# Kernel optimization log

Measured on AMD Instinct MI355X. Metric: run time of the kernel, lower is better.

Reference implementation:

```python
import jax, jax.numpy as jnp
import numpy as np

D = 256        # feature dim
H = 8          # num_heads
HD = D // H    # head dim = 32
G = 16         # graphs in batch
NA = 128       # nodes per graph, side A
NB = 128       # nodes per graph, side B


def setup_inputs() -> dict:
    key = jax.random.key(0)
    ks = jax.random.split(key, 7)
    s = 1.0 / np.sqrt(D)
    A = jax.random.normal(ks[0], (G * NA, D), dtype=jnp.float32)
    B = jax.random.normal(ks[1], (G * NB, D), dtype=jnp.float32)
    batch1 = jnp.repeat(jnp.arange(G, dtype=jnp.int64), NA)
    batch2 = jnp.repeat(jnp.arange(G, dtype=jnp.int64), NB)
    W1 = jax.random.normal(ks[2], (D, D), dtype=jnp.float32) * s
    bias1 = jax.random.normal(ks[3], (D,), dtype=jnp.float32) * s
    W2 = jax.random.normal(ks[4], (D, D), dtype=jnp.float32) * s
    bias2 = jax.random.normal(ks[5], (D,), dtype=jnp.float32) * s
    q = jax.random.normal(ks[6], (HD,), dtype=jnp.float32) * s
    return {"A": A, "batch1": batch1, "B": B, "batch2": batch2,
            "W1": W1, "bias1": bias1, "W2": W2, "bias2": bias2, "q": q}


def reference(A, batch1, B, batch2, W1, bias1, W2, bias2, q):
    # equal-size graphs: counts are uniform, so torch.split == reshape
    g = int(np.asarray(batch1)[-1]) + 1
    nA = A.shape[0] // g
    nB = B.shape[0] // g
    x1 = A @ W1.T + bias1            # [g*nA, D]
    x2 = B @ W2.T + bias2            # [g*nB, D]
    # faithful to torch: raw C-order view [nA, D] -> [H, nA, HD]
    x1 = x1.reshape(g, H, nA, HD)    # [g, H, nA, hd]
    x2 = x2.reshape(g, H, nB, HD)    # [g, H, nB, hd]
    # att[g,h,i,j] = sum_k tanh(x1[g,h,i,k] * x2[g,h,j,k]) * q[k]
    att = jnp.einsum('ghijk,k->ghij',
                     jnp.tanh(x1[:, :, :, None, :] * x2[:, :, None, :, :]), q)
    b2a = jax.nn.softmax(att.mean(axis=3), axis=2)   # [g, H, nA]
    a2b = jax.nn.softmax(att.mean(axis=2), axis=2)   # [g, H, nB]
    A_p = jnp.einsum('ghik,ghi->ghk', x1, b2a).reshape(g, D)
    B_p = jnp.einsum('ghjk,ghj->ghk', x2, a2b).reshape(g, D)
    return jnp.concatenate([A_p, B_p], axis=1)       # [g, 2D]
```

## Files before the change

### kernel.cpp

```cpp
#include <hip/hip_runtime.h>

#define C2L2E 2.8853900817779268f
#define LOG2E 1.4426950408889634f

#define WS_X1   0
#define WS_X2   524288
#define WS_RS   1048576
#define WS_CP   1064960
#define WS_AH   1114112
#define WS_AL   1376256
#define WS_BH   1638400
#define WS_BL   1900544
#define WS_W1H  2162688
#define WS_W1L  2195456
#define WS_W2H  2228224
#define WS_W2L  2260992

#define L_SMAT 0
#define L_COLP 8448
#define L_RED8 8960
#define L_X2   9216
#define L_X1   13312

typedef short bf16x8 __attribute__((ext_vector_type(8)));
typedef float f32x4 __attribute__((ext_vector_type(4)));

__device__ __forceinline__ int swz4(int row, int c4) { return (c4 ^ (row & 7)) << 2; }

__device__ __forceinline__ unsigned short bf16rne(float f) {
    unsigned u = __float_as_uint(f);
    u += 0x7FFF + ((u >> 16) & 1);
    return (unsigned short)(u >> 16);
}
__device__ __forceinline__ float bf16tof(unsigned short h) {
    return __uint_as_float(((unsigned)h) << 16);
}

__global__ __launch_bounds__(512) void k0_convert(
        const float* __restrict__ A, const float* __restrict__ B,
        const float* __restrict__ W1, const float* __restrict__ W2,
        float* __restrict__ ws) {
    const int idx = blockIdx.x * 512 + threadIdx.x;
    const float* src; unsigned short *dh, *dl; int base;
    if (idx < 131072)      { src = A;  dh = (unsigned short*)(ws + WS_AH);  dl = (unsigned short*)(ws + WS_AL);  base = idx; }
    else if (idx < 262144) { src = B;  dh = (unsigned short*)(ws + WS_BH);  dl = (unsigned short*)(ws + WS_BL);  base = idx - 131072; }
    else if (idx < 278528) { src = W1; dh = (unsigned short*)(ws + WS_W1H); dl = (unsigned short*)(ws + WS_W1L); base = idx - 262144; }
    else                   { src = W2; dh = (unsigned short*)(ws + WS_W2H); dl = (unsigned short*)(ws + WS_W2L); base = idx - 278528; }
    float4 v = ((const float4*)src)[base];
    ushort4 h, l;
    h.x = bf16rne(v.x); l.x = bf16rne(v.x - bf16tof(h.x));
    h.y = bf16rne(v.y); l.y = bf16rne(v.y - bf16tof(h.y));
    h.z = bf16rne(v.z); l.z = bf16rne(v.z - bf16tof(h.z));
    h.w = bf16rne(v.w); l.w = bf16rne(v.w - bf16tof(h.w));
    ((ushort4*)dh)[base] = h;
    ((ushort4*)dl)[base] = l;
}

__global__ __launch_bounds__(256) void k1_mfma(
        const float* __restrict__ b1, const float* __restrict__ b2,
        float* __restrict__ ws) {
    const int bid = blockIdx.x, tid = threadIdx.x;
    const int mat = bid >> 7, idx = bid & 127;
    const int r0 = (idx >> 2) * 64, c0 = (idx & 3) * 64;
    const unsigned short* IH = (const unsigned short*)(ws + (mat ? WS_BH : WS_AH));
    const unsigned short* IL = (const unsigned short*)(ws + (mat ? WS_BL : WS_AL));
    const unsigned short* WH = (const unsigned short*)(ws + (mat ? WS_W2H : WS_W1H));
    const unsigned short* WL = (const unsigned short*)(ws + (mat ? WS_W2L : WS_W1L));
    const float* bs = mat ? b2 : b1;
    float* xo = ws + (mat ? WS_X2 : WS_X1);

    const int wv = tid >> 6, lane = tid & 63;
    const int l16 = lane & 15, khi = (lane >> 4) * 8;
    const int row = r0 + wv * 16 + l16;

    f32x4 acc[4];
    #pragma unroll
    for (int nt = 0; nt < 4; ++nt) acc[nt] = (f32x4){0.f, 0.f, 0.f, 0.f};

    const unsigned short* ihp = IH + (size_t)row * 256 + khi;
    const unsigned short* ilp = IL + (size_t)row * 256 + khi;

    for (int kt = 0; kt < 8; ++kt) {
        bf16x8 ah = *(const bf16x8*)(ihp + kt * 32);
        bf16x8 al = *(const bf16x8*)(ilp + kt * 32);
        #pragma unroll
        for (int nt = 0; nt < 4; ++nt) {
            const int cB = c0 + nt * 16 + l16;
            bf16x8 wh = *(const bf16x8*)(WH + (size_t)cB * 256 + kt * 32 + khi);
            bf16x8 wl = *(const bf16x8*)(WL + (size_t)cB * 256 + kt * 32 + khi);
            acc[nt] = __builtin_amdgcn_mfma_f32_16x16x32_bf16(ah, wh, acc[nt], 0, 0, 0);
            acc[nt] = __builtin_amdgcn_mfma_f32_16x16x32_bf16(ah, wl, acc[nt], 0, 0, 0);
            acc[nt] = __builtin_amdgcn_mfma_f32_16x16x32_bf16(al, wh, acc[nt], 0, 0, 0);
        }
    }

    const int rowb = r0 + wv * 16 + (lane >> 4) * 4;
    #pragma unroll
    for (int nt = 0; nt < 4; ++nt) {
        const int col = c0 + nt * 16 + l16;
        const float bb = bs[col];
        #pragma unroll
        for (int rg = 0; rg < 4; ++rg)
            xo[(size_t)(rowb + rg) * 256 + col] = acc[nt][rg] + bb;
    }
}

__global__ __launch_bounds__(512) void k2_att(
        float* __restrict__ ws, const float* __restrict__ q) {
    __shared__ float sm[15360];
    const int tid = threadIdx.x;
    const int gh = blockIdx.x >> 1, s = blockIdx.x & 1;
    float* x2L = sm + L_X2;
    float* x1L = sm + L_X1;

    {
        const float4* src2 = (const float4*)(ws + WS_X2 + (size_t)gh * 4096);
        #pragma unroll
        for (int p = 0; p < 2; ++p) {
            int n = tid + p * 512;
            float4 v = src2[n];
            int ni = n >> 3, c4 = n & 7;
            *(float4*)(x2L + ni * 32 + swz4(ni, c4)) = v;
        }
        const float4* src1 = (const float4*)(ws + WS_X1 + (size_t)gh * 4096 + s * 2048);
        float4 v = src1[tid];
        int nl = tid >> 3, c4 = tid & 7;
        *(float4*)(x1L + nl * 32 + swz4(nl, c4)) = v;
    }
    __syncthreads();

    {
        const int j = tid & 127, iset = tid >> 7;
        float xr[32], qt[32];
        #pragma unroll
        for (int cc = 0; cc < 8; ++cc) {
            float4 v = *(float4*)(x2L + j * 32 + swz4(j, cc));
            xr[cc*4+0] = v.x * C2L2E; xr[cc*4+1] = v.y * C2L2E;
            xr[cc*4+2] = v.z * C2L2E; xr[cc*4+3] = v.w * C2L2E;
            float4 qv = *(const float4*)(q + cc * 4);
            qt[cc*4+0] = -2.f * qv.x; qt[cc*4+1] = -2.f * qv.y;
            qt[cc*4+2] = -2.f * qv.z; qt[cc*4+3] = -2.f * qv.w;
        }
        float colacc = 0.f;
        for (int rr = 0; rr < 16; ++rr) {
            const int r = iset * 16 + rr;
            float a[32];
            #pragma unroll
            for (int cc = 0; cc < 8; ++cc) {
                float4 v = *(float4*)(x1L + r * 32 + swz4(r, cc));
                a[cc*4+0] = v.x; a[cc*4+1] = v.y; a[cc*4+2] = v.z; a[cc*4+3] = v.w;
            }
            float S0 = 0.f, S1 = 0.f;
            #pragma unroll
            for (int kp = 0; kp < 16; ++kp) {
                float p0 = a[2*kp]   * xr[2*kp];
                float p1 = a[2*kp+1] * xr[2*kp+1];
                float d0 = __builtin_amdgcn_exp2f(fminf(p0, 60.f)) + 1.f;
                float d1 = __builtin_amdgcn_exp2f(fminf(p1, 60.f)) + 1.f;
                float rD = __builtin_amdgcn_rcpf(d0 * d1);
                float U  = fmaf(qt[2*kp+1], d0, qt[2*kp] * d1);
                if (kp & 1) S1 = fmaf(U, rD, S1); else S0 = fmaf(U, rD, S0);
            }
            float S = S0 + S1;
            colacc += S;
            sm[L_SMAT + r * 132 + j] = S;
        }
        sm[L_COLP + iset * 128 + j] = colacc;
    }
    __syncthreads();

    if (tid < 256) {
        const int row = tid >> 2, seg = tid & 3;
        float acc = 0.f;
        #pragma unroll
        for (int m = 0; m < 8; ++m) {
            float4 v = *(float4*)(sm + L_SMAT + row * 132 + seg * 32 + m * 4);
            acc += (v.x + v.y) + (v.z + v.w);
        }
        sm[L_RED8 + row * 4 + seg] = acc;
    }
    __syncthreads();
    if (tid < 64) {
        float v = sm[L_RED8 + tid*4] + sm[L_RED8 + tid*4+1]
                + sm[L_RED8 + tid*4+2] + sm[L_RED8 + tid*4+3];
        ws[WS_RS + gh * 128 + s * 64 + tid] = v;
    } else if (tid < 192) {
        const int j = tid - 64;
        ws[WS_CP + (size_t)(gh * 2 + s) * 128 + j] =
            sm[L_COLP + j] + sm[L_COLP + 128 + j] + sm[L_COLP + 256 + j] + sm[L_COLP + 384 + j];
    }
}

__global__ __launch_bounds__(256) void kb_finish(
        const float* __restrict__ ws, float* __restrict__ out) {
    const int gh = blockIdx.x;
    const int g = gh >> 3, h = gh & 7;
    const int tid = threadIdx.x;
    const int side = tid >> 7;
    const int u = tid & 127;
    const int w2 = (u >> 6) & 1;
    const int lane = tid & 63;

    __shared__ float warr[2][128];
    __shared__ float red[4];
    __shared__ float red2[4];
    __shared__ float part[2][4][32];

    float m;
    if (side == 0) {
        m = ws[WS_RS + gh * 128 + u] * 0.0078125f;
    } else {
        m = (ws[WS_CP + (size_t)(gh * 2 + 0) * 128 + u] +
             ws[WS_CP + (size_t)(gh * 2 + 1) * 128 + u]) * 0.0078125f;
    }

    float mx = m;
    #pragma unroll
    for (int d = 32; d >= 1; d >>= 1) mx = fmaxf(mx, __shfl_xor(mx, d));
    if (lane == 0) red[side * 2 + w2] = mx;
    __syncthreads();
    mx = fmaxf(red[side * 2], red[side * 2 + 1]);

    float e = __builtin_amdgcn_exp2f((m - mx) * LOG2E);
    float sme = e;
    #pragma unroll
    for (int d = 32; d >= 1; d >>= 1) sme += __shfl_xor(sme, d);
    if (lane == 0) red2[side * 2 + w2] = sme;
    __syncthreads();
    const float tot = red2[side * 2] + red2[side * 2 + 1];
    warr[side][u] = e * __builtin_amdgcn_rcpf(tot);
    __syncthreads();

    const int k = u & 31, is = u >> 5;
    const float* xt = ws + (side ? WS_X2 : WS_X1) + (size_t)gh * 4096;
    float p = 0.f;
    #pragma unroll 4
    for (int r = 0; r < 32; ++r)
        p = fmaf(xt[(is * 32 + r) * 32 + k], warr[side][is * 32 + r], p);
    part[side][is][k] = p;
    __syncthreads();
    if (u < 32 && side == 0) {
        float o = part[0][0][u] + part[0][1][u] + part[0][2][u] + part[0][3][u];
        out[(size_t)g * 512 + h * 32 + u] = o;
    } else if (u < 32 && side == 1) {
        float o = part[1][0][u] + part[1][1][u] + part[1][2][u] + part[1][3][u];
        out[(size_t)g * 512 + 256 + h * 32 + u] = o;
    }
}

extern "C" void kernel_launch(void* const* d_in, const int* in_sizes, int n_in,
                              void* d_out, int out_size, void* d_ws, size_t ws_size,
                              hipStream_t stream) {
    const float* A  = (const float*)d_in[0];
    const float* B  = (const float*)d_in[2];
    const float* W1 = (const float*)d_in[4];
    const float* b1 = (const float*)d_in[5];
    const float* W2 = (const float*)d_in[6];
    const float* b2 = (const float*)d_in[7];
    const float* q  = (const float*)d_in[8];
    float* ws  = (float*)d_ws;
    float* out = (float*)d_out;

    k0_convert<<<576, 512, 0, stream>>>(A, B, W1, W2, ws);
    k1_mfma<<<256, 256, 0, stream>>>(b1, b2, ws);
    k2_att<<<256, 512, 0, stream>>>(ws, q);
    kb_finish<<<128, 256, 0, stream>>>(ws, out);
}
```

Baseline: 45.38 us.

## Fuse attention and softmax-finish kernels, pre-tile bf16 operands into MFMA fragment layout

The attention and finish kernels are merged into one 1024-thread block per (graph, head). It computes the full 128x128 score tile, does the row and column softmax, and forms the weighted sums from the x1/x2 tiles already in shared memory. This removes one launch and the global round trip for the partial row and column sums. The convert kernel now writes A/B/W hi/lo bf16 data in MFMA-fragment order, so the GEMM reads each fragment as one contiguous 16-byte per-lane load. The trade-off is half as many blocks (128 instead of 256) with larger shared memory, which may lower occupancy during the tanh-heavy phase.

```diff
diff --git a/kernel.cpp b/kernel.cpp
--- a/kernel.cpp
+++ b/kernel.cpp
@@ -5,27 +5,33 @@
 
 #define WS_X1   0
 #define WS_X2   524288
-#define WS_RS   1048576
-#define WS_CP   1064960
-#define WS_AH   1114112
-#define WS_AL   1376256
-#define WS_BH   1638400
-#define WS_BL   1900544
-#define WS_W1H  2162688
-#define WS_W1L  2195456
-#define WS_W2H  2228224
-#define WS_W2L  2260992
-
-#define L_SMAT 0
-#define L_COLP 8448
-#define L_RED8 8960
-#define L_X2   9216
-#define L_X1   13312
+#define WS_AH   1048576
+#define WS_AL   1310720
+#define WS_BH   1572864
+#define WS_BL   1835008
+#define WS_W1H  2097152
+#define WS_W1L  2129920
+#define WS_W2H  2162688
+#define WS_W2L  2195456
+
+#define L_X2    0
+#define L_X1    4096
+#define L_SMAT  8192
+#define L_COLP  25088
+#define L_RED8  27136
+#define L_RSUM  28160
+#define L_CSUM  28288
+#define L_WARR  28416
+#define L_REDM  28672
+#define L_PART  28680
 
 typedef short bf16x8 __attribute__((ext_vector_type(8)));
 typedef float f32x4 __attribute__((ext_vector_type(4)));
 
 __device__ __forceinline__ int swz4(int row, int c4) { return (c4 ^ (row & 7)) << 2; }
+__device__ __forceinline__ int swzf(int row, int k) {
+    return (((k >> 2) ^ (row & 7)) << 2) | (k & 3);
+}
 
 __device__ __forceinline__ unsigned short bf16rne(float f) {
     unsigned u = __float_as_uint(f);
@@ -36,24 +42,34 @@
     return __uint_as_float(((unsigned)h) << 16);
 }
 
-__global__ __launch_bounds__(512) void k0_convert(
+__global__ __launch_bounds__(256) void k0_convert(
         const float* __restrict__ A, const float* __restrict__ B,
         const float* __restrict__ W1, const float* __restrict__ W2,
         float* __restrict__ ws) {
-    const int idx = blockIdx.x * 512 + threadIdx.x;
-    const float* src; unsigned short *dh, *dl; int base;
-    if (idx < 131072)      { src = A;  dh = (unsigned short*)(ws + WS_AH);  dl = (unsigned short*)(ws + WS_AL);  base = idx; }
-    else if (idx < 262144) { src = B;  dh = (unsigned short*)(ws + WS_BH);  dl = (unsigned short*)(ws + WS_BL);  base = idx - 131072; }
-    else if (idx < 278528) { src = W1; dh = (unsigned short*)(ws + WS_W1H); dl = (unsigned short*)(ws + WS_W1L); base = idx - 262144; }
-    else                   { src = W2; dh = (unsigned short*)(ws + WS_W2H); dl = (unsigned short*)(ws + WS_W2L); base = idx - 278528; }
-    float4 v = ((const float4*)src)[base];
-    ushort4 h, l;
-    h.x = bf16rne(v.x); l.x = bf16rne(v.x - bf16tof(h.x));
-    h.y = bf16rne(v.y); l.y = bf16rne(v.y - bf16tof(h.y));
-    h.z = bf16rne(v.z); l.z = bf16rne(v.z - bf16tof(h.z));
-    h.w = bf16rne(v.w); l.w = bf16rne(v.w - bf16tof(h.w));
-    ((ushort4*)dh)[base] = h;
-    ((ushort4*)dl)[base] = l;
+    const int t = blockIdx.x * 256 + threadIdx.x;
+    const float* src; unsigned short *dh, *dl; int tl;
+    if (t < 65536)       { src = A;  dh = (unsigned short*)(ws + WS_AH);  dl = (unsigned short*)(ws + WS_AL);  tl = t; }
+    else if (t < 131072) { src = B;  dh = (unsigned short*)(ws + WS_BH);  dl = (unsigned short*)(ws + WS_BL);  tl = t - 65536; }
+    else if (t < 139264) { src = W1; dh = (unsigned short*)(ws + WS_W1H); dl = (unsigned short*)(ws + WS_W1L); tl = t - 131072; }
+    else                 { src = W2; dh = (unsigned short*)(ws + WS_W2H); dl = (unsigned short*)(ws + WS_W2L); tl = t - 139264; }
+    const int lane = tl & 63, kt = (tl >> 6) & 7, rt = tl >> 9;
+    const int row = rt * 16 + (lane & 15);
+    const int col = kt * 32 + (lane >> 4) * 8;
+    float4 v0 = *(const float4*)(src + (size_t)row * 256 + col);
+    float4 v1 = *(const float4*)(src + (size_t)row * 256 + col + 4);
+    ushort4 h0, h1, l0, l1;
+    h0.x = bf16rne(v0.x); l0.x = bf16rne(v0.x - bf16tof(h0.x));
+    h0.y = bf16rne(v0.y); l0.y = bf16rne(v0.y - bf16tof(h0.y));
+    h0.z = bf16rne(v0.z); l0.z = bf16rne(v0.z - bf16tof(h0.z));
+    h0.w = bf16rne(v0.w); l0.w = bf16rne(v0.w - bf16tof(h0.w));
+    h1.x = bf16rne(v1.x); l1.x = bf16rne(v1.x - bf16tof(h1.x));
+    h1.y = bf16rne(v1.y); l1.y = bf16rne(v1.y - bf16tof(h1.y));
+    h1.z = bf16rne(v1.z); l1.z = bf16rne(v1.z - bf16tof(h1.z));
+    h1.w = bf16rne(v1.w); l1.w = bf16rne(v1.w - bf16tof(h1.w));
+    ((ushort4*)dh)[tl * 2]     = h0;
+    ((ushort4*)dh)[tl * 2 + 1] = h1;
+    ((ushort4*)dl)[tl * 2]     = l0;
+    ((ushort4*)dl)[tl * 2 + 1] = l1;
 }
 
 __global__ __launch_bounds__(256) void k1_mfma(
@@ -64,30 +80,27 @@
     const int r0 = (idx >> 2) * 64, c0 = (idx & 3) * 64;
     const unsigned short* IH = (const unsigned short*)(ws + (mat ? WS_BH : WS_AH));
     const unsigned short* IL = (const unsigned short*)(ws + (mat ? WS_BL : WS_AL));
-    const unsigned short* WH = (const unsigned short*)(ws + (mat ? WS_W2H : WS_W1H));
-    const unsigned short* WL = (const unsigned short*)(ws + (mat ? WS_W2L : WS_W1L));
+    const unsigned short* WHp = (const unsigned short*)(ws + (mat ? WS_W2H : WS_W1H));
+    const unsigned short* WLp = (const unsigned short*)(ws + (mat ? WS_W2L : WS_W1L));
     const float* bs = mat ? b2 : b1;
     float* xo = ws + (mat ? WS_X2 : WS_X1);
 
     const int wv = tid >> 6, lane = tid & 63;
-    const int l16 = lane & 15, khi = (lane >> 4) * 8;
-    const int row = r0 + wv * 16 + l16;
+    const int rt = (idx >> 2) * 4 + wv;
+    const int ct0 = (idx & 3) * 4;
 
     f32x4 acc[4];
     #pragma unroll
     for (int nt = 0; nt < 4; ++nt) acc[nt] = (f32x4){0.f, 0.f, 0.f, 0.f};
 
-    const unsigned short* ihp = IH + (size_t)row * 256 + khi;
-    const unsigned short* ilp = IL + (size_t)row * 256 + khi;
-
     for (int kt = 0; kt < 8; ++kt) {
-        bf16x8 ah = *(const bf16x8*)(ihp + kt * 32);
-        bf16x8 al = *(const bf16x8*)(ilp + kt * 32);
+        bf16x8 ah = *(const bf16x8*)(IH + ((size_t)(rt * 8 + kt) * 64 + lane) * 8);
+        bf16x8 al = *(const bf16x8*)(IL + ((size_t)(rt * 8 + kt) * 64 + lane) * 8);
         #pragma unroll
         for (int nt = 0; nt < 4; ++nt) {
-            const int cB = c0 + nt * 16 + l16;
-            bf16x8 wh = *(const bf16x8*)(WH + (size_t)cB * 256 + kt * 32 + khi);
-            bf16x8 wl = *(const bf16x8*)(WL + (size_t)cB * 256 + kt * 32 + khi);
+            const int ct = ct0 + nt;
+            bf16x8 wh = *(const bf16x8*)(WHp + ((size_t)(ct * 8 + kt) * 64 + lane) * 8);
+            bf16x8 wl = *(const bf16x8*)(WLp + ((size_t)(ct * 8 + kt) * 64 + lane) * 8);
             acc[nt] = __builtin_amdgcn_mfma_f32_16x16x32_bf16(ah, wh, acc[nt], 0, 0, 0);
             acc[nt] = __builtin_amdgcn_mfma_f32_16x16x32_bf16(ah, wl, acc[nt], 0, 0, 0);
             acc[nt] = __builtin_amdgcn_mfma_f32_16x16x32_bf16(al, wh, acc[nt], 0, 0, 0);
@@ -95,6 +108,7 @@
     }
 
     const int rowb = r0 + wv * 16 + (lane >> 4) * 4;
+    const int l16 = lane & 15;
     #pragma unroll
     for (int nt = 0; nt < 4; ++nt) {
         const int col = c0 + nt * 16 + l16;
@@ -105,146 +119,157 @@
     }
 }
 
-__global__ __launch_bounds__(512) void k2_att(
-        float* __restrict__ ws, const float* __restrict__ q) {
-    __shared__ float sm[15360];
+__global__ __launch_bounds__(1024) void k23_att_finish(
+        float* __restrict__ ws, const float* __restrict__ q,
+        float* __restrict__ out) {
+    __shared__ float sm[28936];
     const int tid = threadIdx.x;
-    const int gh = blockIdx.x >> 1, s = blockIdx.x & 1;
+    const int gh = blockIdx.x;
+    const int g = gh >> 3, h = gh & 7;
     float* x2L = sm + L_X2;
     float* x1L = sm + L_X1;
 
     {
         const float4* src2 = (const float4*)(ws + WS_X2 + (size_t)gh * 4096);
-        #pragma unroll
-        for (int p = 0; p < 2; ++p) {
-            int n = tid + p * 512;
-            float4 v = src2[n];
-            int ni = n >> 3, c4 = n & 7;
-            *(float4*)(x2L + ni * 32 + swz4(ni, c4)) = v;
-        }
-        const float4* src1 = (const float4*)(ws + WS_X1 + (size_t)gh * 4096 + s * 2048);
-        float4 v = src1[tid];
-        int nl = tid >> 3, c4 = tid & 7;
-        *(float4*)(x1L + nl * 32 + swz4(nl, c4)) = v;
+        const float4* src1 = (const float4*)(ws + WS_X1 + (size_t)gh * 4096);
+        float4 v = src2[tid];
+        float4 w = src1[tid];
+        const int ni = tid >> 3, c4 = tid & 7;
+        *(float4*)(x2L + ni * 32 + swz4(ni, c4)) = v;
+        *(float4*)(x1L + ni * 32 + swz4(ni, c4)) = w;
     }
     __syncthreads();
 
     {
-        const int j = tid & 127, iset = tid >> 7;
-        float xr[32], qt[32];
+        const int jp = tid & 63, iset = tid >> 6;
+        float xr0[32], xr1[32], qt[32];
         #pragma unroll
         for (int cc = 0; cc < 8; ++cc) {
-            float4 v = *(float4*)(x2L + j * 32 + swz4(j, cc));
-            xr[cc*4+0] = v.x * C2L2E; xr[cc*4+1] = v.y * C2L2E;
-            xr[cc*4+2] = v.z * C2L2E; xr[cc*4+3] = v.w * C2L2E;
+            float4 v = *(float4*)(x2L + jp * 32 + swz4(jp, cc));
+            xr0[cc*4+0] = v.x * C2L2E; xr0[cc*4+1] = v.y * C2L2E;
+            xr0[cc*4+2] = v.z * C2L2E; xr0[cc*4+3] = v.w * C2L2E;
+            float4 w = *(float4*)(x2L + (jp + 64) * 32 + swz4(jp + 64, cc));
+            xr1[cc*4+0] = w.x * C2L2E; xr1[cc*4+1] = w.y * C2L2E;
+            xr1[cc*4+2] = w.z * C2L2E; xr1[cc*4+3] = w.w * C2L2E;
             float4 qv = *(const float4*)(q + cc * 4);
             qt[cc*4+0] = -2.f * qv.x; qt[cc*4+1] = -2.f * qv.y;
             qt[cc*4+2] = -2.f * qv.z; qt[cc*4+3] = -2.f * qv.w;
         }
-        float colacc = 0.f;
-        for (int rr = 0; rr < 16; ++rr) {
-            const int r = iset * 16 + rr;
-            float a[32];
+        float colacc0 = 0.f, colacc1 = 0.f;
+        for (int rr = 0; rr < 8; ++rr) {
+            const int r = iset * 8 + rr;
+            float Sa = 0.f, Sb = 0.f;
             #pragma unroll
             for (int cc = 0; cc < 8; ++cc) {
-                float4 v = *(float4*)(x1L + r * 32 + swz4(r, cc));
-                a[cc*4+0] = v.x; a[cc*4+1] = v.y; a[cc*4+2] = v.z; a[cc*4+3] = v.w;
+                float4 a4 = *(float4*)(x1L + r * 32 + swz4(r, cc));
+                {
+                    float p0 = a4.x * xr0[cc*4+0], p1 = a4.y * xr0[cc*4+1];
+                    float d0 = __builtin_amdgcn_exp2f(fminf(p0, 60.f)) + 1.f;
+                    float d1 = __builtin_amdgcn_exp2f(fminf(p1, 60.f)) + 1.f;
+                    float rD = __builtin_amdgcn_rcpf(d0 * d1);
+                    float U  = fmaf(qt[cc*4+1], d0, qt[cc*4+0] * d1);
+                    Sa = fmaf(U, rD, Sa);
+                    p0 = a4.z * xr0[cc*4+2]; p1 = a4.w * xr0[cc*4+3];
+                    d0 = __builtin_amdgcn_exp2f(fminf(p0, 60.f)) + 1.f;
+                    d1 = __builtin_amdgcn_exp2f(fminf(p1, 60.f)) + 1.f;
+                    rD = __builtin_amdgcn_rcpf(d0 * d1);
+                    U  = fmaf(qt[cc*4+3], d0, qt[cc*4+2] * d1);
+                    Sa = fmaf(U, rD, Sa);
+                }
+                {
+                    float p0 = a4.x * xr1[cc*4+0], p1 = a4.y * xr1[cc*4+1];
+                    float d0 = __builtin_amdgcn_exp2f(fminf(p0, 60.f)) + 1.f;
+                    float d1 = __builtin_amdgcn_exp2f(fminf(p1, 60.f)) + 1.f;
+                    float rD = __builtin_amdgcn_rcpf(d0 * d1);
+                    float U  = fmaf(qt[cc*4+1], d0, qt[cc*4+0] * d1);
+                    Sb = fmaf(U, rD, Sb);
+                    p0 = a4.z * xr1[cc*4+2]; p1 = a4.w * xr1[cc*4+3];
+                    d0 = __builtin_amdgcn_exp2f(fminf(p0, 60.f)) + 1.f;
+                    d1 = __builtin_amdgcn_exp2f(fminf(p1, 60.f)) + 1.f;
+                    rD = __builtin_amdgcn_rcpf(d0 * d1);
+                    U  = fmaf(qt[cc*4+3], d0, qt[cc*4+2] * d1);
+                    Sb = fmaf(U, rD, Sb);
+                }
             }
-            float S0 = 0.f, S1 = 0.f;
-            #pragma unroll
-            for (int kp = 0; kp < 16; ++kp) {
-                float p0 = a[2*kp]   * xr[2*kp];
-                float p1 = a[2*kp+1] * xr[2*kp+1];
-                float d0 = __builtin_amdgcn_exp2f(fminf(p0, 60.f)) + 1.f;
-                float d1 = __builtin_amdgcn_exp2f(fminf(p1, 60.f)) + 1.f;
-                float rD = __builtin_amdgcn_rcpf(d0 * d1);
-                float U  = fmaf(qt[2*kp+1], d0, qt[2*kp] * d1);
-                if (kp & 1) S1 = fmaf(U, rD, S1); else S0 = fmaf(U, rD, S0);
-            }
-            float S = S0 + S1;
-            colacc += S;
-            sm[L_SMAT + r * 132 + j] = S;
-        }
-        sm[L_COLP + iset * 128 + j] = colacc;
-    }
-    __syncthreads();
-
-    if (tid < 256) {
-        const int row = tid >> 2, seg = tid & 3;
+            sm[L_SMAT + r * 132 + jp]      = Sa;
+            sm[L_SMAT + r * 132 + jp + 64] = Sb;
+            colacc0 += Sa; colacc1 += Sb;
+        }
+        sm[L_COLP + iset * 128 + jp]      = colacc0;
+        sm[L_COLP + iset * 128 + jp + 64] = colacc1;
+    }
+    __syncthreads();
+
+    {
+        const int row = tid >> 3, seg = tid & 7;
         float acc = 0.f;
         #pragma unroll
-        for (int m = 0; m < 8; ++m) {
-            float4 v = *(float4*)(sm + L_SMAT + row * 132 + seg * 32 + m * 4);
+        for (int m = 0; m < 4; ++m) {
+            float4 v = *(float4*)(sm + L_SMAT + row * 132 + seg * 16 + m * 4);
             acc += (v.x + v.y) + (v.z + v.w);
         }
-        sm[L_RED8 + row * 4 + seg] = acc;
-    }
-    __syncthreads();
-    if (tid < 64) {
-        float v = sm[L_RED8 + tid*4] + sm[L_RED8 + tid*4+1]
-                + sm[L_RED8 + tid*4+2] + sm[L_RED8 + tid*4+3];
-        ws[WS_RS + gh * 128 + s * 64 + tid] = v;
-    } else if (tid < 192) {
-        const int j = tid - 64;
-        ws[WS_CP + (size_t)(gh * 2 + s) * 128 + j] =
-            sm[L_COLP + j] + sm[L_COLP + 128 + j] + sm[L_COLP + 256 + j] + sm[L_COLP + 384 + j];
-    }
-}
-
-__global__ __launch_bounds__(256) void kb_finish(
-        const float* __restrict__ ws, float* __restrict__ out) {
-    const int gh = blockIdx.x;
-    const int g = gh >> 3, h = gh & 7;
-    const int tid = threadIdx.x;
-    const int side = tid >> 7;
-    const int u = tid & 127;
-    const int w2 = (u >> 6) & 1;
-    const int lane = tid & 63;
-
-    __shared__ float warr[2][128];
-    __shared__ float red[4];
-    __shared__ float red2[4];
-    __shared__ float part[2][4][32];
-
-    float m;
-    if (side == 0) {
-        m = ws[WS_RS + gh * 128 + u] * 0.0078125f;
-    } else {
-        m = (ws[WS_CP + (size_t)(gh * 2 + 0) * 128 + u] +
-             ws[WS_CP + (size_t)(gh * 2 + 1) * 128 + u]) * 0.0078125f;
-    }
-
-    float mx = m;
-    #pragma unroll
-    for (int d = 32; d >= 1; d >>= 1) mx = fmaxf(mx, __shfl_xor(mx, d));
-    if (lane == 0) red[side * 2 + w2] = mx;
-    __syncthreads();
-    mx = fmaxf(red[side * 2], red[side * 2 + 1]);
-
-    float e = __builtin_amdgcn_exp2f((m - mx) * LOG2E);
-    float sme = e;
-    #pragma unroll
-    for (int d = 32; d >= 1; d >>= 1) sme += __shfl_xor(sme, d);
-    if (lane == 0) red2[side * 2 + w2] = sme;
-    __syncthreads();
-    const float tot = red2[side * 2] + red2[side * 2 + 1];
-    warr[side][u] = e * __builtin_amdgcn_rcpf(tot);
-    __syncthreads();
-
-    const int k = u & 31, is = u >> 5;
-    const float* xt = ws + (side ? WS_X2 : WS_X1) + (size_t)gh * 4096;
-    float p = 0.f;
-    #pragma unroll 4
-    for (int r = 0; r < 32; ++r)
-        p = fmaf(xt[(is * 32 + r) * 32 + k], warr[side][is * 32 + r], p);
-    part[side][is][k] = p;
-    __syncthreads();
-    if (u < 32 && side == 0) {
-        float o = part[0][0][u] + part[0][1][u] + part[0][2][u] + part[0][3][u];
-        out[(size_t)g * 512 + h * 32 + u] = o;
-    } else if (u < 32 && side == 1) {
-        float o = part[1][0][u] + part[1][1][u] + part[1][2][u] + part[1][3][u];
-        out[(size_t)g * 512 + 256 + h * 32 + u] = o;
+        sm[L_RED8 + row * 8 + seg] = acc;
+    }
+    __syncthreads();
+    if (tid < 128) {
+        float s = 0.f;
+        #pragma unroll
+        for (int m = 0; m < 8; ++m) s += sm[L_RED8 + tid * 8 + m];
+        sm[L_RSUM + tid] = s;
+        float cs = 0.f;
+        #pragma unroll
+        for (int is = 0; is < 16; ++is) cs += sm[L_COLP + is * 128 + tid];
+        sm[L_CSUM + tid] = cs;
+    }
+    __syncthreads();
+
+    const int side = tid >> 7, u = tid & 127;
+    const int w2b = (u >> 6) & 1, lane = tid & 63;
+    float m = 0.f, e = 0.f;
+    if (tid < 256) {
+        m = (side ? sm[L_CSUM + u] : sm[L_RSUM + u]) * 0.0078125f;
+        float mx = m;
+        #pragma unroll
+        for (int d = 32; d >= 1; d >>= 1) mx = fmaxf(mx, __shfl_xor(mx, d));
+        if (lane == 0) sm[L_REDM + side * 2 + w2b] = mx;
+    }
+    __syncthreads();
+    if (tid < 256) {
+        float mx = fmaxf(sm[L_REDM + side * 2], sm[L_REDM + side * 2 + 1]);
+        e = __builtin_amdgcn_exp2f((m - mx) * LOG2E);
+        float sme = e;
+        #pragma unroll
+        for (int d = 32; d >= 1; d >>= 1) sme += __shfl_xor(sme, d);
+        if (lane == 0) sm[L_REDM + 4 + side * 2 + w2b] = sme;
+    }
+    __syncthreads();
+    if (tid < 256) {
+        float tot = sm[L_REDM + 4 + side * 2] + sm[L_REDM + 4 + side * 2 + 1];
+        sm[L_WARR + side * 128 + u] = e * __builtin_amdgcn_rcpf(tot);
+    }
+    __syncthreads();
+
+    if (tid < 256) {
+        const int k = u & 31, is = u >> 5;
+        const float* xt = side ? x2L : x1L;
+        float p = 0.f;
+        #pragma unroll 4
+        for (int r2 = 0; r2 < 32; ++r2) {
+            const int ni = is * 32 + r2;
+            p = fmaf(xt[ni * 32 + swzf(ni, k)], sm[L_WARR + side * 128 + ni], p);
+        }
+        sm[L_PART + side * 128 + is * 32 + k] = p;
+    }
+    __syncthreads();
+    if (tid < 32) {
+        float o = sm[L_PART + tid] + sm[L_PART + 32 + tid]
+                + sm[L_PART + 64 + tid] + sm[L_PART + 96 + tid];
+        out[(size_t)g * 512 + h * 32 + tid] = o;
+    } else if (tid >= 64 && tid < 96) {
+        const int kk = tid - 64;
+        float o = sm[L_PART + 128 + kk] + sm[L_PART + 160 + kk]
+                + sm[L_PART + 192 + kk] + sm[L_PART + 224 + kk];
+        out[(size_t)g * 512 + 256 + h * 32 + kk] = o;
     }
 }
 
@@ -261,8 +286,7 @@
     float* ws  = (float*)d_ws;
     float* out = (float*)d_out;
 
-    k0_convert<<<576, 512, 0, stream>>>(A, B, W1, W2, ws);
+    k0_convert<<<576, 256, 0, stream>>>(A, B, W1, W2, ws);
     k1_mfma<<<256, 256, 0, stream>>>(b1, b2, ws);
-    k2_att<<<256, 512, 0, stream>>>(ws, q);
-    kb_finish<<<128, 256, 0, stream>>>(ws, out);
-}
+    k23_att_finish<<<128, 1024, 0, stream>>>(ws, q, out);
+}
```

New measurement: 52.84 us. 16.4% more time.
